# Performance work log

Hardware: AMD Instinct MI355X
Metric: run time of the kernel (lower is better)

## Reference

```python
import jax, jax.numpy as jnp
import numpy as np
import math

B, L, D, H, R = 2, 1024, 768, 12, 256
DH = D // H  # 64


def layernorm(x, g, b, eps=1e-5):
    mu = jnp.mean(x, axis=-1, keepdims=True)
    var = jnp.mean((x - mu) ** 2, axis=-1, keepdims=True)
    return (x - mu) / jnp.sqrt(var + eps) * g + b


def setup_inputs() -> dict:
    key = jax.random.key(0)
    ks = jax.random.split(key, 8)
    x = jax.random.normal(ks[0], (B, L, D), dtype=jnp.float32)
    conv_w = jax.random.normal(ks[1], (D, 3), dtype=jnp.float32) * 0.3   # depthwise k=3
    conv_b = jnp.zeros((D,), jnp.float32)
    ln_g = jnp.ones((D,), jnp.float32)
    ln_b = jnp.zeros((D,), jnp.float32)
    qkv_w = jax.random.normal(ks[2], (3 * D, D), dtype=jnp.float32) / math.sqrt(D)
    qkv_b = jnp.zeros((3 * D,), jnp.float32)
    bn_w1 = jax.random.normal(ks[3], (R, D), dtype=jnp.float32) / math.sqrt(D)
    bn_w2 = jax.random.normal(ks[4], (H * 5, R), dtype=jnp.float32) / math.sqrt(R)
    temperature = jnp.ones((1,), jnp.float32) * 0.5
    proj_w = jax.random.normal(ks[5], (D, D), dtype=jnp.float32) / math.sqrt(D)
    proj_b = jnp.zeros((D,), jnp.float32)
    mn_g = jnp.ones((DH,), jnp.float32)
    mn_b = jnp.zeros((DH,), jnp.float32)
    return {"x": x, "conv_w": conv_w, "conv_b": conv_b, "ln_g": ln_g, "ln_b": ln_b,
            "qkv_w": qkv_w, "qkv_b": qkv_b, "bn_w1": bn_w1, "bn_w2": bn_w2,
            "temperature": temperature, "proj_w": proj_w, "proj_b": proj_b,
            "mn_g": mn_g, "mn_b": mn_b}


def reference(x, conv_w, conv_b, ln_g, ln_b, qkv_w, qkv_b, bn_w1, bn_w2,
              temperature, proj_w, proj_b, mn_g, mn_b):
    Bx, Lx, Dx = x.shape
    # causal depthwise conv1d (kernel 3, pad 2 then drop last 2 == left-pad 2)
    xp = jnp.pad(x, ((0, 0), (2, 0), (0, 0)))
    conv = (xp[:, 0:Lx] * conv_w[:, 0] + xp[:, 1:Lx + 1] * conv_w[:, 1]
            + xp[:, 2:Lx + 2] * conv_w[:, 2]) + conv_b
    x_conv = x + conv
    xn = layernorm(x_conv, ln_g, ln_b)

    qkv = xn @ qkv_w.T + qkv_b
    q, k, v = jnp.split(qkv, 3, axis=-1)

    params = (jax.nn.silu(xn @ bn_w1.T) @ bn_w2.T).reshape(Bx, Lx, H, 5)
    sem_amp = jax.nn.sigmoid(params[..., 0])
    sem_phase = jnp.tanh(params[..., 1]) * math.pi
    ctx_amp = jax.nn.sigmoid(params[..., 2])
    ctx_phase = jnp.tanh(params[..., 3]) * math.pi
    decay = 0.3 + 0.65 * jax.nn.sigmoid(params[..., 4])  # (B,L,H)
    gate = jax.nn.sigmoid(sem_amp * ctx_amp * jnp.cos(sem_phase - ctx_phase) * temperature[0])

    q_f = (jax.nn.elu(q) + 1.0).reshape(Bx, Lx, H, DH)
    k_f = (jax.nn.elu(k) + 1.0).reshape(Bx, Lx, H, DH)
    v_f = v.reshape(Bx, Lx, H, DH)

    one_minus = 1.0 - decay                                    # (B,L,H)
    kv_input = jnp.einsum('blhd,blhe->blhde', k_f, v_f)        # (B,L,H,dh,dh)
    kv_input = jnp.clip(kv_input * (gate * one_minus)[..., None, None], -5.0, 5.0)

    df = jnp.exp(jnp.cumsum(jnp.log(decay), axis=1))           # (B,L,H)
    safe_df = df + 1e-8
    kv_states = jnp.cumsum(kv_input / safe_df[..., None, None], axis=1) * df[..., None, None]

    z = jnp.cumsum(k_f * one_minus[..., None] / safe_df[..., None], axis=1) * df[..., None]
    z = jnp.clip(z, -10000.0, 10000.0)

    out_num = jnp.einsum('blhd,blhde->blhe', q_f, kv_states)   # (B,L,H,dh)
    den = jnp.sum(q_f * z, axis=-1, keepdims=True) + 0.0001
    out = layernorm(out_num / den, mn_g, mn_b)                 # (B,L,H,dh)

    y = out.reshape(Bx, Lx, Dx) @ proj_w.T + proj_b
    return y, gate
```

## Files before the change

kernel.cpp:

```cpp
#include <hip/hip_runtime.h>
#include <math.h>

#define LL 1024
#define DD 768
#define HH 12
#define CL 16
#define NC 64
#define NBH 24

typedef __bf16 bf16x8 __attribute__((ext_vector_type(8)));
typedef __bf16 bf16x4 __attribute__((ext_vector_type(4)));
typedef float floatx4 __attribute__((ext_vector_type(4)));

typedef const void __attribute__((address_space(1)))* gas_ptr;
typedef void __attribute__((address_space(3)))* las_ptr;

__device__ __forceinline__ void gl_lds16(const void* g, void* s) {
  __builtin_amdgcn_global_load_lds((gas_ptr)g, (las_ptr)s, 16, 0, 0);
}

__device__ __forceinline__ float wave_sum64(float v) {
#pragma unroll
  for (int off = 32; off; off >>= 1) v += __shfl_xor(v, off, 64);
  return v;
}

__device__ __forceinline__ float sigm(float x) { return 1.0f / (1.0f + expf(-x)); }
__device__ __forceinline__ float clamp5(float x) {
  return __builtin_amdgcn_fmed3f(x, -5.f, 5.f);
}

__global__ __launch_bounds__(256) void prep_kernel(
    const float* __restrict__ x, const float* __restrict__ cw,
    const float* __restrict__ cb, const float* __restrict__ g,
    const float* __restrict__ bta, __bf16* __restrict__ xn,
    const float* __restrict__ qkvw, const float* __restrict__ bnw1,
    const float* __restrict__ projw, const float* __restrict__ w2,
    __bf16* __restrict__ wqb, __bf16* __restrict__ dp, __bf16* __restrict__ dw2) {
  if (blockIdx.x >= 2048) {
    int i = (blockIdx.x - 2048) * 256 + threadIdx.x;
    if (i >= 647168) return;
    bf16x4 o;
    if (i >= 638976) {
      int off = i - 638976;
      if (off < 3840) {
        float4 v = ((const float4*)w2)[off];
        o[0] = (__bf16)v.x; o[1] = (__bf16)v.y; o[2] = (__bf16)v.z; o[3] = (__bf16)v.w;
      } else {
        o[0] = (__bf16)0.f; o[1] = (__bf16)0.f; o[2] = (__bf16)0.f; o[3] = (__bf16)0.f;
      }
      ((bf16x4*)dw2)[off] = o;
      return;
    }
    const float* s; __bf16* d; int off;
    if (i < 442368)      { s = qkvw;  d = wqb;  off = i; }
    else if (i < 491520) { s = bnw1;  d = wqb;  off = i; }
    else                 { s = projw; d = dp;   off = i - 491520; }
    int soff = (i < 442368) ? i : (i < 491520 ? i - 442368 : off);
    float4 v = ((const float4*)s)[soff];
    o[0] = (__bf16)v.x; o[1] = (__bf16)v.y; o[2] = (__bf16)v.z; o[3] = (__bf16)v.w;
    ((bf16x4*)d)[off] = o;
    return;
  }
  int row = blockIdx.x;
  int l = row & (LL - 1);
  const float* xr = x + (size_t)row * DD;
  __shared__ float red[16];
  float vals[3];
  float s = 0.f, ss = 0.f;
#pragma unroll
  for (int i = 0; i < 3; i++) {
    int d = threadIdx.x + i * 256;
    float x0 = xr[d];
    float xm1 = (l >= 1) ? xr[d - DD] : 0.f;
    float xm2 = (l >= 2) ? xr[d - 2 * DD] : 0.f;
    float c = xm2 * cw[d * 3 + 0] + xm1 * cw[d * 3 + 1] + x0 * cw[d * 3 + 2] + cb[d];
    float v = x0 + c;
    vals[i] = v; s += v; ss += v * v;
  }
  s = wave_sum64(s); ss = wave_sum64(ss);
  int wid = threadIdx.x >> 6;
  if ((threadIdx.x & 63) == 0) { red[wid * 2] = s; red[wid * 2 + 1] = ss; }
  __syncthreads();
  if (threadIdx.x == 0) {
    red[8] = red[0] + red[2] + red[4] + red[6];
    red[9] = red[1] + red[3] + red[5] + red[7];
  }
  __syncthreads();
  float mu = red[8] * (1.f / 768.f);
  float var = red[9] * (1.f / 768.f) - mu * mu;
  float inv = rsqrtf(var + 1e-5f);
  __bf16* xo = xn + (size_t)row * DD;
#pragma unroll
  for (int i = 0; i < 3; i++) {
    int d = threadIdx.x + i * 256;
    xo[d] = (__bf16)((vals[i] - mu) * inv * g[d] + bta[d]);
  }
}

template <int BM, int MODE, bool HASBIAS, bool OUTBF>
__global__ __launch_bounds__(256) void gemm_mfma_kernel(
    const __bf16* __restrict__ A, const __bf16* __restrict__ Bw,
    const float* __restrict__ bias, void* __restrict__ Cv, void* __restrict__ C2,
    int M, int N, int K) {
  constexpr int MI = BM / 32;
  __shared__ __attribute__((aligned(16))) __bf16 As[BM * 64];
  __shared__ __attribute__((aligned(16))) __bf16 Bs[128 * 64];
  int m0 = blockIdx.y * BM, n0 = blockIdx.x * 128;
  int tid = threadIdx.x;
  int w = tid >> 6, lane = tid & 63;
  int wm = w >> 1, wn = w & 1;
  int quad = lane >> 4, l16 = lane & 15;

  int lrow = lane >> 3;
  int lchunk = (lane & 7) ^ lrow;
  int R0 = w * 8;

  floatx4 acc[MI][4];
#pragma unroll
  for (int i = 0; i < MI; i++)
#pragma unroll
    for (int j = 0; j < 4; j++) acc[i][j] = (floatx4)0.f;

  for (int k0 = 0; k0 < K; k0 += 64) {
    __syncthreads();
#pragma unroll
    for (int r = 0; r < BM / 32; r++) {
      int row = r * 32 + R0 + lrow;
      gl_lds16(A + (size_t)(m0 + row) * K + k0 + lchunk * 8, &As[(r * 32 + R0) * 64]);
    }
#pragma unroll
    for (int r = 0; r < 4; r++) {
      int row = r * 32 + R0 + lrow;
      gl_lds16(Bw + (size_t)(n0 + row) * K + k0 + lchunk * 8, &Bs[(r * 32 + R0) * 64]);
    }
    __syncthreads();
#pragma unroll
    for (int s = 0; s < 2; s++) {
      bf16x8 af[MI], bfr[4];
      int csw = (s << 2) + quad;
#pragma unroll
      for (int i = 0; i < MI; i++) {
        int m = wm * (BM / 2) + i * 16 + l16;
        af[i] = *(const bf16x8*)&As[m * 64 + (csw ^ (l16 & 7)) * 8];
      }
#pragma unroll
      for (int j = 0; j < 4; j++) {
        int n = wn * 64 + j * 16 + l16;
        bfr[j] = *(const bf16x8*)&Bs[n * 64 + (csw ^ (l16 & 7)) * 8];
      }
#pragma unroll
      for (int i = 0; i < MI; i++)
#pragma unroll
        for (int j = 0; j < 4; j++)
          acc[i][j] = __builtin_amdgcn_mfma_f32_16x16x32_bf16(af[i], bfr[j], acc[i][j], 0, 0, 0);
    }
  }
#pragma unroll
  for (int j = 0; j < 4; j++) {
    int gcol = n0 + wn * 64 + j * 16 + l16;
    if (MODE == 3) {
      if (gcol < 2304) {
        float bv = bias[gcol];
        bool isqk = gcol < 1536;
#pragma unroll
        for (int i = 0; i < MI; i++) {
          int grow = m0 + wm * (BM / 2) + i * 16 + quad * 4;
#pragma unroll
          for (int r = 0; r < 4; r++) {
            float v = acc[i][j][r] + bv;
            if (isqk) v = (v > 0.f) ? v + 1.f : expf(v);
            ((float*)Cv)[(size_t)(grow + r) * 2304 + gcol] = v;
          }
        }
      } else {
        int hcol = gcol - 2304;
#pragma unroll
        for (int i = 0; i < MI; i++) {
          int grow = m0 + wm * (BM / 2) + i * 16 + quad * 4;
#pragma unroll
          for (int r = 0; r < 4; r++) {
            float v = acc[i][j][r];
            v = v / (1.f + expf(-v));
            ((__bf16*)C2)[(size_t)(grow + r) * 256 + hcol] = (__bf16)v;
          }
        }
      }
    } else {
      float bv = HASBIAS ? bias[gcol] : 0.f;
#pragma unroll
      for (int i = 0; i < MI; i++) {
        int grow = m0 + wm * (BM / 2) + i * 16 + quad * 4;
#pragma unroll
        for (int r = 0; r < 4; r++) {
          float v = acc[i][j][r] + bv;
          if (OUTBF) ((__bf16*)Cv)[(size_t)(grow + r) * N + gcol] = (__bf16)v;
          else       ((float*)Cv)[(size_t)(grow + r) * N + gcol] = v;
        }
      }
    }
  }
}

__global__ __launch_bounds__(256) void params_df_kernel(
    const float* __restrict__ pp, const float* __restrict__ temp,
    float* __restrict__ gate, float* __restrict__ dec, float* __restrict__ dfb) {
  int bh = blockIdx.x;
  int b = bh / HH, h = bh - b * HH;
  int tid = threadIdx.x;
  int lane = tid & 63, wid = tid >> 6;
  float tv = temp[0];
  const float PI = 3.14159265358979323846f;
  double ls[4];
  double lsum = 0.0;
#pragma unroll
  for (int i = 0; i < 4; i++) {
    int l = tid * 4 + i;
    int row = (b << 10) + l;
    const float* p = pp + (size_t)row * 128 + h * 5;
    float p0 = p[0], p1 = p[1], p2 = p[2], p3 = p[3], p4 = p[4];
    float sa = sigm(p0);
    float sp = tanhf(p1) * PI;
    float ca = sigm(p2);
    float cp = tanhf(p3) * PI;
    float dc = 0.3f + 0.65f * sigm(p4);
    float gt = sigm(sa * ca * cosf(sp - cp) * tv);
    gate[row * HH + h] = gt;
    dec[(bh << 10) + l] = dc;
    lsum += (double)logf(dc);
    ls[i] = lsum;
  }
  double run = lsum;
#pragma unroll
  for (int off = 1; off < 64; off <<= 1) {
    double n = __shfl_up(run, off, 64);
    if (lane >= off) run += n;
  }
  __shared__ double wsum[4];
  if (lane == 63) wsum[wid] = run;
  __syncthreads();
  double wexcl = 0.0;
  for (int k = 0; k < wid; k++) wexcl += wsum[k];
  double excl = wexcl + run - lsum;
  float* dfo = dfb + (bh << 10) + tid * 4;
#pragma unroll
  for (int i = 0; i < 4; i++) dfo[i] = expf((float)(excl + ls[i]));
}

__global__ __launch_bounds__(256) void scan_phase1(
    const float* __restrict__ qkv, const float* __restrict__ dec,
    const float* __restrict__ df, const float* __restrict__ gate,
    __bf16* __restrict__ kvcs, float* __restrict__ zcs, float* __restrict__ Aarr) {
  int blk = blockIdx.x;
  int bh = blk >> 6, c = blk & (NC - 1);
  int b = bh / HH, h = bh - b * HH;
  int tid = threadIdx.x;
  int w = tid >> 6, e = tid & 63;
  int t0 = c * CL;
  __shared__ __attribute__((aligned(16))) float kbuf[CL][64];
  __shared__ __attribute__((aligned(16))) float vbuf[CL][64];
  __shared__ float sbuf[CL][4];
  const float* base = qkv + ((size_t)(b * LL + t0)) * 2304 + h * 64;
  {
    int t = (w << 2) + (e >> 4);
    int col = (e & 15) << 2;
    gl_lds16(base + (size_t)t * 2304 + 768 + col, &kbuf[w << 2][0]);
    gl_lds16(base + (size_t)t * 2304 + 1536 + col, &vbuf[w << 2][0]);
  }
  if (tid < CL) {
    int t = t0 + tid;
    float a = dec[bh * LL + t];
    float d = df[bh * LL + t];
    float r = d / (d + 1e-8f);
    float g = gate[(b * LL + t) * HH + h];
    sbuf[tid][0] = a; sbuf[tid][1] = r; sbuf[tid][2] = g * (1.f - a);
    sbuf[tid][3] = (1.f - a) * r;
  }
  __syncthreads();
  float KV[16];
#pragma unroll
  for (int d = 0; d < 16; d++) KV[d] = 0.f;
  float z = 0.f, A = 1.f;
  for (int t = 0; t < CL; t++) {
    float a = sbuf[t][0], r = sbuf[t][1], cs = sbuf[t][2], w1r = sbuf[t][3];
    float vc = vbuf[t][e] * cs;
    A *= a;
#pragma unroll
    for (int d4 = 0; d4 < 4; d4++) {
      float4 k4 = *(const float4*)&kbuf[t][(w << 4) + (d4 << 2)];
      float kr[4] = {k4.x, k4.y, k4.z, k4.w};
#pragma unroll
      for (int j = 0; j < 4; j++) {
        float u = clamp5(kr[j] * vc);
        KV[(d4 << 2) + j] = fmaf(a, KV[(d4 << 2) + j], r * u);
      }
    }
    z = fmaf(a, z, kbuf[t][e] * w1r);
  }
  __bf16* kvo = kvcs + (size_t)blk * 4096 + (w << 4) * 64 + e;
#pragma unroll
  for (int d = 0; d < 16; d++) kvo[d * 64] = (__bf16)KV[d];
  if (w == 0) zcs[blk * 64 + e] = z;
  if (tid == 0) Aarr[blk] = A;
}

__global__ __launch_bounds__(256) void combine_kernel(
    const float* __restrict__ Aarr, __bf16* __restrict__ kv, float* __restrict__ z) {
  int g = blockIdx.x * 256 + threadIdx.x;
  if (g < NBH * 4096) {
    int bh = g >> 12, idx = g & 4095;
    const float* Ap = Aarr + bh * NC;
    __bf16* p = kv + (size_t)bh * NC * 4096 + idx;
    float carry = 0.f;
#pragma unroll 8
    for (int c = 0; c < NC; c++) {
      float endv = (float)p[(size_t)c * 4096];
      p[(size_t)c * 4096] = (__bf16)carry;
      carry = fmaf(Ap[c], carry, endv);
    }
  } else {
    int g2 = g - NBH * 4096;
    if (g2 >= NBH * 64) return;
    int bh = g2 >> 6, idx = g2 & 63;
    const float* Ap = Aarr + bh * NC;
    float* p = z + bh * NC * 64 + idx;
    float carry = 0.f;
#pragma unroll 8
    for (int c = 0; c < NC; c++) {
      float endv = p[c * 64];
      p[c * 64] = carry;
      carry = fmaf(Ap[c], carry, endv);
    }
  }
}

__global__ __launch_bounds__(256) void scan_phase3(
    const float* __restrict__ qkv, const float* __restrict__ dec,
    const float* __restrict__ df, const float* __restrict__ gate,
    const __bf16* __restrict__ kvcs, const float* __restrict__ zcs,
    const float* __restrict__ mng, const float* __restrict__ mnb,
    __bf16* __restrict__ att) {
  int blk = blockIdx.x;
  int bh = blk >> 6, c = blk & (NC - 1);
  int b = bh / HH, h = bh - b * HH;
  int tid = threadIdx.x;
  int w = tid >> 6, e = tid & 63;
  int t0 = c * CL;
  __shared__ __attribute__((aligned(16))) float qbuf[CL][64];
  __shared__ __attribute__((aligned(16))) float kbuf[CL][64];
  __shared__ __attribute__((aligned(16))) float vbuf[CL][64];
  __shared__ float sbuf[CL][4];
  __shared__ float pbuf[CL][4][64];
  const float* base = qkv + ((size_t)(b * LL + t0)) * 2304 + h * 64;
  {
    int t = (w << 2) + (e >> 4);
    int col = (e & 15) << 2;
    gl_lds16(base + (size_t)t * 2304 + col, &qbuf[w << 2][0]);
    gl_lds16(base + (size_t)t * 2304 + 768 + col, &kbuf[w << 2][0]);
    gl_lds16(base + (size_t)t * 2304 + 1536 + col, &vbuf[w << 2][0]);
  }
  if (tid < CL) {
    int t = t0 + tid;
    float a = dec[bh * LL + t];
    float d = df[bh * LL + t];
    float r = d / (d + 1e-8f);
    float g = gate[(b * LL + t) * HH + h];
    sbuf[tid][0] = a; sbuf[tid][1] = r; sbuf[tid][2] = g * (1.f - a);
    sbuf[tid][3] = (1.f - a) * r;
  }
  float KV[16];
  const __bf16* kvi = kvcs + (size_t)blk * 4096 + (w << 4) * 64 + e;
#pragma unroll
  for (int d = 0; d < 16; d++) KV[d] = (float)kvi[d * 64];
  float z = zcs[blk * 64 + e];
  float zsnap[4];
  __syncthreads();
  for (int t = 0; t < CL; t++) {
    float a = sbuf[t][0], r = sbuf[t][1], cs = sbuf[t][2], w1r = sbuf[t][3];
    float vc = vbuf[t][e] * cs;
    float onp = 0.f;
#pragma unroll
    for (int d4 = 0; d4 < 4; d4++) {
      float4 k4 = *(const float4*)&kbuf[t][(w << 4) + (d4 << 2)];
      float4 q4 = *(const float4*)&qbuf[t][(w << 4) + (d4 << 2)];
      float kr[4] = {k4.x, k4.y, k4.z, k4.w};
      float qr[4] = {q4.x, q4.y, q4.z, q4.w};
#pragma unroll
      for (int j = 0; j < 4; j++) {
        float u = clamp5(kr[j] * vc);
        float nv = fmaf(a, KV[(d4 << 2) + j], r * u);
        KV[(d4 << 2) + j] = nv;
        onp = fmaf(qr[j], nv, onp);
      }
    }
    pbuf[t][w][e] = onp;
    z = fmaf(a, z, kbuf[t][e] * w1r);
    if ((t >> 2) == w) zsnap[t & 3] = z;
  }
  __syncthreads();
  float mg = mng[e], mb = mnb[e];
#pragma unroll
  for (int i = 0; i < 4; i++) {
    int t = (w << 2) + i;
    float on = pbuf[t][0][e] + pbuf[t][1][e] + pbuf[t][2][e] + pbuf[t][3][e];
    float zc = __builtin_amdgcn_fmed3f(zsnap[i], -10000.f, 10000.f);
    float qe = qbuf[t][e];
    float s0 = qe * zc, s1 = on, s2 = on * on;
#pragma unroll
    for (int off = 32; off; off >>= 1) {
      s0 += __shfl_xor(s0, off, 64);
      s1 += __shfl_xor(s1, off, 64);
      s2 += __shfl_xor(s2, off, 64);
    }
    float den = s0 + 1e-4f;
    float idn = 1.f / den;
    float o = on * idn;
    float mu = s1 * idn * (1.f / 64.f);
    float E2 = s2 * idn * idn * (1.f / 64.f);
    float var = E2 - mu * mu;
    float outv = (o - mu) * rsqrtf(var + 1e-5f) * mg + mb;
    att[((size_t)(b * LL + t0 + t)) * DD + h * 64 + e] = (__bf16)outv;
  }
}

extern "C" void kernel_launch(void* const* d_in, const int* in_sizes, int n_in,
                              void* d_out, int out_size, void* d_ws, size_t ws_size,
                              hipStream_t stream) {
  (void)in_sizes; (void)n_in; (void)out_size; (void)ws_size;
  const float* x           = (const float*)d_in[0];
  const float* conv_w      = (const float*)d_in[1];
  const float* conv_b      = (const float*)d_in[2];
  const float* ln_g        = (const float*)d_in[3];
  const float* ln_b        = (const float*)d_in[4];
  const float* qkv_w       = (const float*)d_in[5];
  const float* qkv_b       = (const float*)d_in[6];
  const float* bn_w1       = (const float*)d_in[7];
  const float* bn_w2       = (const float*)d_in[8];
  const float* temperature = (const float*)d_in[9];
  const float* proj_w      = (const float*)d_in[10];
  const float* proj_b      = (const float*)d_in[11];
  const float* mn_g        = (const float*)d_in[12];
  const float* mn_b        = (const float*)d_in[13];

  float* y    = (float*)d_out;
  float* gate = y + 2 * 1024 * 768;

  char* ws = (char*)d_ws;
  __bf16* xn_bf   = (__bf16*)(ws);
  __bf16* att_bf  = xn_bf;
  float*  qkva    = (float*)(ws + 3145728);
  __bf16* hbuf_bf = (__bf16*)(ws + 22020096);
  float*  pp      = (float*)(ws + 23068672);
  float*  dec     = (float*)(ws + 24117248);
  float*  dfb     = (float*)(ws + 24215552);
  __bf16* kvcs    = (__bf16*)(ws + 24313856);
  __bf16* wqb_bf  = (__bf16*)(ws + 24313856);
  float*  zcs     = (float*)(ws + 36896768);
  float*  Aarr    = (float*)(ws + 37289984);
  __bf16* projw_bf= (__bf16*)(ws + 37296128);
  __bf16* w2p_bf  = (__bf16*)(ws + 38475776);

  prep_kernel<<<4576, 256, 0, stream>>>(x, conv_w, conv_b, ln_g, ln_b, xn_bf,
                                        qkv_w, bn_w1, proj_w, bn_w2,
                                        wqb_bf, projw_bf, w2p_bf);

  gemm_mfma_kernel<64, 3, true, false><<<dim3(20, 32), 256, 0, stream>>>(
      xn_bf, wqb_bf, qkv_b, qkva, hbuf_bf, 2048, 2560, 768);

  gemm_mfma_kernel<64, 0, false, false><<<dim3(1, 32), 256, 0, stream>>>(
      hbuf_bf, w2p_bf, nullptr, pp, nullptr, 2048, 128, 256);

  params_df_kernel<<<NBH, 256, 0, stream>>>(pp, temperature, gate, dec, dfb);

  scan_phase1<<<NBH * NC, 256, 0, stream>>>(qkva, dec, dfb, gate, kvcs, zcs, Aarr);

  combine_kernel<<<390, 256, 0, stream>>>(Aarr, kvcs, zcs);

  scan_phase3<<<NBH * NC, 256, 0, stream>>>(qkva, dec, dfb, gate, kvcs, zcs,
                                            mn_g, mn_b, att_bf);

  gemm_mfma_kernel<64, 0, true, false><<<dim3(6, 32), 256, 0, stream>>>(
      att_bf, projw_bf, proj_b, y, nullptr, 2048, 768, 768);
}
```

Baseline: 176.1 us.

## Store QKV activations in bf16, remap GEMM blocks, and shrink scan LDS

The QKV GEMM epilogue now writes q/k/v as bf16 instead of fp32, and both scan kernels load bf16 tiles into LDS, which halves the traffic on the largest intermediate buffer. GEMM launches become 1D grids with a block-index remap that spreads consecutive blocks across M rows, which may change L2 and XCD locality. scan_phase3 processes the chunk in two halves so its partial-sum LDS buffer shrinks by half, and both scan kernels request an occupancy of 6 blocks through launch bounds. The cost is reduced precision for q/k/v and an extra barrier per chunk.

```diff
diff --git a/kernel.cpp b/kernel.cpp
--- a/kernel.cpp
+++ b/kernel.cpp
@@ -98,15 +98,19 @@
   }
 }
 
-template <int BM, int MODE, bool HASBIAS, bool OUTBF>
+template <int BM, int NY, int MODE, bool HASBIAS, bool OUTBF>
 __global__ __launch_bounds__(256) void gemm_mfma_kernel(
     const __bf16* __restrict__ A, const __bf16* __restrict__ Bw,
     const float* __restrict__ bias, void* __restrict__ Cv, void* __restrict__ C2,
     int M, int N, int K) {
   constexpr int MI = BM / 32;
+  constexpr int NYG = NY / 8;
   __shared__ __attribute__((aligned(16))) __bf16 As[BM * 64];
   __shared__ __attribute__((aligned(16))) __bf16 Bs[128 * 64];
-  int m0 = blockIdx.y * BM, n0 = blockIdx.x * 128;
+  int id = blockIdx.x;
+  int by = (id & 7) * NYG + ((id >> 3) % NYG);
+  int bx = (id >> 3) / NYG;
+  int m0 = by * BM, n0 = bx * 128;
   int tid = threadIdx.x;
   int w = tid >> 6, lane = tid & 63;
   int wm = w >> 1, wn = w & 1;
@@ -170,7 +174,7 @@
           for (int r = 0; r < 4; r++) {
             float v = acc[i][j][r] + bv;
             if (isqk) v = (v > 0.f) ? v + 1.f : expf(v);
-            ((float*)Cv)[(size_t)(grow + r) * 2304 + gcol] = v;
+            ((__bf16*)Cv)[(size_t)(grow + r) * 2304 + gcol] = (__bf16)v;
           }
         }
       } else {
@@ -247,8 +251,8 @@
   for (int i = 0; i < 4; i++) dfo[i] = expf((float)(excl + ls[i]));
 }
 
-__global__ __launch_bounds__(256) void scan_phase1(
-    const float* __restrict__ qkv, const float* __restrict__ dec,
+__global__ __launch_bounds__(256, 6) void scan_phase1(
+    const __bf16* __restrict__ qkv, const float* __restrict__ dec,
     const float* __restrict__ df, const float* __restrict__ gate,
     __bf16* __restrict__ kvcs, float* __restrict__ zcs, float* __restrict__ Aarr) {
   int blk = blockIdx.x;
@@ -257,15 +261,16 @@
   int tid = threadIdx.x;
   int w = tid >> 6, e = tid & 63;
   int t0 = c * CL;
-  __shared__ __attribute__((aligned(16))) float kbuf[CL][64];
-  __shared__ __attribute__((aligned(16))) float vbuf[CL][64];
+  __shared__ __attribute__((aligned(16))) __bf16 kbuf[CL][64];
+  __shared__ __attribute__((aligned(16))) __bf16 vbuf[CL][64];
   __shared__ float sbuf[CL][4];
-  const float* base = qkv + ((size_t)(b * LL + t0)) * 2304 + h * 64;
   {
-    int t = (w << 2) + (e >> 4);
-    int col = (e & 15) << 2;
-    gl_lds16(base + (size_t)t * 2304 + 768 + col, &kbuf[w << 2][0]);
-    gl_lds16(base + (size_t)t * 2304 + 1536 + col, &vbuf[w << 2][0]);
+    int trow = ((w & 1) << 3) + (e >> 3);
+    int chunk = e & 7;
+    int sec = (w < 2) ? 1 : 2;
+    const __bf16* gp = qkv + ((size_t)(b * LL + t0 + trow) * 2304 + sec * 768 + h * 64 + chunk * 8);
+    void* dst = (w < 2) ? (void*)&kbuf[(w & 1) << 3][0] : (void*)&vbuf[(w & 1) << 3][0];
+    gl_lds16(gp, dst);
   }
   if (tid < CL) {
     int t = t0 + tid;
@@ -283,19 +288,21 @@
   float z = 0.f, A = 1.f;
   for (int t = 0; t < CL; t++) {
     float a = sbuf[t][0], r = sbuf[t][1], cs = sbuf[t][2], w1r = sbuf[t][3];
-    float vc = vbuf[t][e] * cs;
+    float vc = (float)vbuf[t][e] * cs;
     A *= a;
-#pragma unroll
-    for (int d4 = 0; d4 < 4; d4++) {
-      float4 k4 = *(const float4*)&kbuf[t][(w << 4) + (d4 << 2)];
-      float kr[4] = {k4.x, k4.y, k4.z, k4.w};
-#pragma unroll
-      for (int j = 0; j < 4; j++) {
-        float u = clamp5(kr[j] * vc);
-        KV[(d4 << 2) + j] = fmaf(a, KV[(d4 << 2) + j], r * u);
-      }
-    }
-    z = fmaf(a, z, kbuf[t][e] * w1r);
+    bf16x8 k0 = *(const bf16x8*)&kbuf[t][w << 4];
+    bf16x8 k1 = *(const bf16x8*)&kbuf[t][(w << 4) + 8];
+#pragma unroll
+    for (int j = 0; j < 8; j++) {
+      float u = clamp5((float)k0[j] * vc);
+      KV[j] = fmaf(a, KV[j], r * u);
+    }
+#pragma unroll
+    for (int j = 0; j < 8; j++) {
+      float u = clamp5((float)k1[j] * vc);
+      KV[8 + j] = fmaf(a, KV[8 + j], r * u);
+    }
+    z = fmaf(a, z, (float)kbuf[t][e] * w1r);
   }
   __bf16* kvo = kvcs + (size_t)blk * 4096 + (w << 4) * 64 + e;
 #pragma unroll
@@ -334,8 +341,8 @@
   }
 }
 
-__global__ __launch_bounds__(256) void scan_phase3(
-    const float* __restrict__ qkv, const float* __restrict__ dec,
+__global__ __launch_bounds__(256, 6) void scan_phase3(
+    const __bf16* __restrict__ qkv, const float* __restrict__ dec,
     const float* __restrict__ df, const float* __restrict__ gate,
     const __bf16* __restrict__ kvcs, const float* __restrict__ zcs,
     const float* __restrict__ mng, const float* __restrict__ mnb,
@@ -346,18 +353,21 @@
   int tid = threadIdx.x;
   int w = tid >> 6, e = tid & 63;
   int t0 = c * CL;
-  __shared__ __attribute__((aligned(16))) float qbuf[CL][64];
-  __shared__ __attribute__((aligned(16))) float kbuf[CL][64];
-  __shared__ __attribute__((aligned(16))) float vbuf[CL][64];
+  __shared__ __attribute__((aligned(16))) __bf16 qbuf[CL][64];
+  __shared__ __attribute__((aligned(16))) __bf16 kbuf[CL][64];
+  __shared__ __attribute__((aligned(16))) __bf16 vbuf[CL][64];
   __shared__ float sbuf[CL][4];
-  __shared__ float pbuf[CL][4][64];
-  const float* base = qkv + ((size_t)(b * LL + t0)) * 2304 + h * 64;
+  __shared__ float pbuf[8][4][64];
   {
-    int t = (w << 2) + (e >> 4);
-    int col = (e & 15) << 2;
-    gl_lds16(base + (size_t)t * 2304 + col, &qbuf[w << 2][0]);
-    gl_lds16(base + (size_t)t * 2304 + 768 + col, &kbuf[w << 2][0]);
-    gl_lds16(base + (size_t)t * 2304 + 1536 + col, &vbuf[w << 2][0]);
+    int trow = ((w & 1) << 3) + (e >> 3);
+    int chunk = e & 7;
+    size_t rowbase = (size_t)(b * LL + t0 + trow) * 2304 + h * 64 + chunk * 8;
+    if (w < 2) {
+      gl_lds16(qkv + rowbase, &qbuf[(w & 1) << 3][0]);
+      gl_lds16(qkv + rowbase + 768, &kbuf[(w & 1) << 3][0]);
+    } else {
+      gl_lds16(qkv + rowbase + 1536, &vbuf[(w & 1) << 3][0]);
+    }
   }
   if (tid < CL) {
     int t = t0 + tid;
@@ -374,52 +384,62 @@
   for (int d = 0; d < 16; d++) KV[d] = (float)kvi[d * 64];
   float z = zcs[blk * 64 + e];
   float zsnap[4];
+  float mg = mng[e], mb = mnb[e];
   __syncthreads();
-  for (int t = 0; t < CL; t++) {
-    float a = sbuf[t][0], r = sbuf[t][1], cs = sbuf[t][2], w1r = sbuf[t][3];
-    float vc = vbuf[t][e] * cs;
-    float onp = 0.f;
-#pragma unroll
-    for (int d4 = 0; d4 < 4; d4++) {
-      float4 k4 = *(const float4*)&kbuf[t][(w << 4) + (d4 << 2)];
-      float4 q4 = *(const float4*)&qbuf[t][(w << 4) + (d4 << 2)];
-      float kr[4] = {k4.x, k4.y, k4.z, k4.w};
-      float qr[4] = {q4.x, q4.y, q4.z, q4.w};
-#pragma unroll
-      for (int j = 0; j < 4; j++) {
-        float u = clamp5(kr[j] * vc);
-        float nv = fmaf(a, KV[(d4 << 2) + j], r * u);
-        KV[(d4 << 2) + j] = nv;
-        onp = fmaf(qr[j], nv, onp);
-      }
-    }
-    pbuf[t][w][e] = onp;
-    z = fmaf(a, z, kbuf[t][e] * w1r);
-    if ((t >> 2) == w) zsnap[t & 3] = z;
-  }
-  __syncthreads();
-  float mg = mng[e], mb = mnb[e];
-#pragma unroll
-  for (int i = 0; i < 4; i++) {
-    int t = (w << 2) + i;
-    float on = pbuf[t][0][e] + pbuf[t][1][e] + pbuf[t][2][e] + pbuf[t][3][e];
-    float zc = __builtin_amdgcn_fmed3f(zsnap[i], -10000.f, 10000.f);
-    float qe = qbuf[t][e];
-    float s0 = qe * zc, s1 = on, s2 = on * on;
-#pragma unroll
-    for (int off = 32; off; off >>= 1) {
-      s0 += __shfl_xor(s0, off, 64);
-      s1 += __shfl_xor(s1, off, 64);
-      s2 += __shfl_xor(s2, off, 64);
-    }
-    float den = s0 + 1e-4f;
-    float idn = 1.f / den;
-    float o = on * idn;
-    float mu = s1 * idn * (1.f / 64.f);
-    float E2 = s2 * idn * idn * (1.f / 64.f);
-    float var = E2 - mu * mu;
-    float outv = (o - mu) * rsqrtf(var + 1e-5f) * mg + mb;
-    att[((size_t)(b * LL + t0 + t)) * DD + h * 64 + e] = (__bf16)outv;
+#pragma unroll
+  for (int half = 0; half < 2; half++) {
+    for (int tt = 0; tt < 8; tt++) {
+      int t = (half << 3) + tt;
+      float a = sbuf[t][0], r = sbuf[t][1], cs = sbuf[t][2], w1r = sbuf[t][3];
+      float vc = (float)vbuf[t][e] * cs;
+      float onp = 0.f;
+      bf16x8 k0 = *(const bf16x8*)&kbuf[t][w << 4];
+      bf16x8 k1 = *(const bf16x8*)&kbuf[t][(w << 4) + 8];
+      bf16x8 q0 = *(const bf16x8*)&qbuf[t][w << 4];
+      bf16x8 q1 = *(const bf16x8*)&qbuf[t][(w << 4) + 8];
+#pragma unroll
+      for (int j = 0; j < 8; j++) {
+        float u = clamp5((float)k0[j] * vc);
+        float nv = fmaf(a, KV[j], r * u);
+        KV[j] = nv;
+        onp = fmaf((float)q0[j], nv, onp);
+      }
+#pragma unroll
+      for (int j = 0; j < 8; j++) {
+        float u = clamp5((float)k1[j] * vc);
+        float nv = fmaf(a, KV[8 + j], r * u);
+        KV[8 + j] = nv;
+        onp = fmaf((float)q1[j], nv, onp);
+      }
+      pbuf[tt][w][e] = onp;
+      z = fmaf(a, z, (float)kbuf[t][e] * w1r);
+      if ((tt >> 1) == w) zsnap[(half << 1) | (tt & 1)] = z;
+    }
+    __syncthreads();
+#pragma unroll
+    for (int i = 0; i < 2; i++) {
+      int tt = (w << 1) + i;
+      int t = (half << 3) + tt;
+      float on = pbuf[tt][0][e] + pbuf[tt][1][e] + pbuf[tt][2][e] + pbuf[tt][3][e];
+      float zc = __builtin_amdgcn_fmed3f(zsnap[(half << 1) | i], -10000.f, 10000.f);
+      float qe = (float)qbuf[t][e];
+      float s0 = qe * zc, s1 = on, s2 = on * on;
+#pragma unroll
+      for (int off = 32; off; off >>= 1) {
+        s0 += __shfl_xor(s0, off, 64);
+        s1 += __shfl_xor(s1, off, 64);
+        s2 += __shfl_xor(s2, off, 64);
+      }
+      float den = s0 + 1e-4f;
+      float idn = 1.f / den;
+      float o = on * idn;
+      float mu = s1 * idn * (1.f / 64.f);
+      float E2 = s2 * idn * idn * (1.f / 64.f);
+      float var = E2 - mu * mu;
+      float outv = (o - mu) * rsqrtf(var + 1e-5f) * mg + mb;
+      att[((size_t)(b * LL + t0 + t)) * DD + h * 64 + e] = (__bf16)outv;
+    }
+    if (half == 0) __syncthreads();
   }
 }
 
@@ -448,26 +468,26 @@
   char* ws = (char*)d_ws;
   __bf16* xn_bf   = (__bf16*)(ws);
   __bf16* att_bf  = xn_bf;
-  float*  qkva    = (float*)(ws + 3145728);
-  __bf16* hbuf_bf = (__bf16*)(ws + 22020096);
-  float*  pp      = (float*)(ws + 23068672);
-  float*  dec     = (float*)(ws + 24117248);
-  float*  dfb     = (float*)(ws + 24215552);
-  __bf16* kvcs    = (__bf16*)(ws + 24313856);
-  __bf16* wqb_bf  = (__bf16*)(ws + 24313856);
-  float*  zcs     = (float*)(ws + 36896768);
-  float*  Aarr    = (float*)(ws + 37289984);
-  __bf16* projw_bf= (__bf16*)(ws + 37296128);
-  __bf16* w2p_bf  = (__bf16*)(ws + 38475776);
+  __bf16* qkva    = (__bf16*)(ws + 3145728);
+  __bf16* hbuf_bf = (__bf16*)(ws + 12582912);
+  float*  pp      = (float*)(ws + 13631488);
+  float*  dec     = (float*)(ws + 14680064);
+  float*  dfb     = (float*)(ws + 14778368);
+  __bf16* kvcs    = (__bf16*)(ws + 14876672);
+  __bf16* wqb_bf  = (__bf16*)(ws + 14876672);
+  float*  zcs     = (float*)(ws + 27459584);
+  float*  Aarr    = (float*)(ws + 27852800);
+  __bf16* projw_bf= (__bf16*)(ws + 27858944);
+  __bf16* w2p_bf  = (__bf16*)(ws + 29038592);
 
   prep_kernel<<<4576, 256, 0, stream>>>(x, conv_w, conv_b, ln_g, ln_b, xn_bf,
                                         qkv_w, bn_w1, proj_w, bn_w2,
                                         wqb_bf, projw_bf, w2p_bf);
 
-  gemm_mfma_kernel<64, 3, true, false><<<dim3(20, 32), 256, 0, stream>>>(
+  gemm_mfma_kernel<64, 32, 3, true, false><<<640, 256, 0, stream>>>(
       xn_bf, wqb_bf, qkv_b, qkva, hbuf_bf, 2048, 2560, 768);
 
-  gemm_mfma_kernel<64, 0, false, false><<<dim3(1, 32), 256, 0, stream>>>(
+  gemm_mfma_kernel<64, 32, 0, false, false><<<32, 256, 0, stream>>>(
       hbuf_bf, w2p_bf, nullptr, pp, nullptr, 2048, 128, 256);
 
   params_df_kernel<<<NBH, 256, 0, stream>>>(pp, temperature, gate, dec, dfb);
@@ -479,6 +499,6 @@
   scan_phase3<<<NBH * NC, 256, 0, stream>>>(qkva, dec, dfb, gate, kvcs, zcs,
                                             mn_g, mn_b, att_bf);
 
-  gemm_mfma_kernel<64, 0, true, false><<<dim3(6, 32), 256, 0, stream>>>(
+  gemm_mfma_kernel<64, 32, 0, true, false><<<192, 256, 0, stream>>>(
       att_bf, projw_bf, proj_b, y, nullptr, 2048, 768, 768);
 }
```

New measurement: 180.0 us. 2.2% more time.
